# Optimization experiments

Hardware: AMD Instinct MI355X
Metric: run time of the kernel (lower is better)

Reference implementation:

```python
import jax, jax.numpy as jnp
import numpy as np

B, LQ, LK, D, H, DFF = 2, 2048, 2048, 512, 8, 2048


def _xavier(key, shape):
    fan_in, fan_out = shape[0], shape[1]
    lim = float(np.sqrt(6.0 / (fan_in + fan_out)))
    return jax.random.uniform(key, shape, jnp.float32, -lim, lim)


def setup_inputs() -> dict:
    key = jax.random.key(0)
    ks = jax.random.split(key, 8)
    return {
        "inputs": jax.random.normal(ks[0], (B, LQ, D), jnp.float32),
        "encoder_x": jax.random.normal(ks[1], (B, LK, D), jnp.float32),
        "Wq": _xavier(ks[2], (D, D)),
        "Wk": _xavier(ks[3], (D, D)),
        "Wv": _xavier(ks[4], (D, D)),
        "ln1_g": jnp.ones((D,), jnp.float32),
        "ln1_b": jnp.zeros((D,), jnp.float32),
        "W1": jax.random.normal(ks[5], (D, DFF), jnp.float32) * 0.02,
        "b1": jnp.zeros((DFF,), jnp.float32),
        "W2": jax.random.normal(ks[6], (DFF, D), jnp.float32) * 0.02,
        "b2": jnp.zeros((D,), jnp.float32),
        "ln2_g": jnp.ones((D,), jnp.float32),
        "ln2_b": jnp.zeros((D,), jnp.float32),
        "n_heads": H,
    }


def _layer_norm(x, g, b, eps=1e-5):
    mu = jnp.mean(x, axis=-1, keepdims=True)
    var = jnp.var(x, axis=-1, keepdims=True)
    return (x - mu) * jax.lax.rsqrt(var + eps) * g + b


def reference(inputs, encoder_x, Wq, Wk, Wv, ln1_g, ln1_b, W1, b1, W2, b2, ln2_g, ln2_b, n_heads):
    b, lq, d = inputs.shape
    lk = encoder_x.shape[1]
    hd = d // n_heads
    q = (inputs @ Wq).reshape(b, lq, n_heads, hd)
    k = (encoder_x @ Wk).reshape(b, lk, n_heads, hd)
    v = (encoder_x @ Wv).reshape(b, lk, n_heads, hd)
    # scores: [b, h, lq, lk]; scale by sqrt(head_dim) as in source
    scores = jnp.einsum("bqhd,bkhd->bhqk", q, k) / jnp.sqrt(jnp.asarray(hd, q.dtype))
    attn = jax.nn.softmax(scores, axis=-1)
    o = jnp.einsum("bhqk,bkhd->bqhd", attn, v).reshape(b, lq, d)
    out = _layer_norm(o + inputs, ln1_g, ln1_b)
    ff = jax.nn.relu(out @ W1 + b1) @ W2 + b2
    return _layer_norm(ff + out, ln2_g, ln2_b)
```

## Files before the change

kernel.cpp:

```cpp
#include <hip/hip_runtime.h>

typedef __bf16 bf16_t;
typedef __bf16 bf16x8 __attribute__((ext_vector_type(8)));
typedef __bf16 bf16x4 __attribute__((ext_vector_type(4)));
typedef float f32x4 __attribute__((ext_vector_type(4)));
typedef float f32x16 __attribute__((ext_vector_type(16)));
typedef unsigned int u32;
typedef unsigned int u32x2 __attribute__((ext_vector_type(2)));

#define GLB_AS(p) ((const __attribute__((address_space(1))) unsigned int*)(p))
#define LDS_AS(p) ((__attribute__((address_space(3))) unsigned int*)(p))

#define SPLIT_ROWS 32768
#define KLD 68
#define VLD 44

__global__ void prep_kernel(const float* __restrict__ inputs, bf16_t* __restrict__ Xb, float scaleQ,
                            const float* __restrict__ encx, bf16_t* __restrict__ Eb,
                            const float* __restrict__ Wq, const float* __restrict__ Wk,
                            const float* __restrict__ Wv, const float* __restrict__ W1,
                            const float* __restrict__ W2, bf16_t* __restrict__ Wqkvt,
                            bf16_t* __restrict__ W1t, bf16_t* __restrict__ W2t)
{
    __shared__ float tile[32][33];
    const int bid = blockIdx.x;
    const int tid = threadIdx.x;
    if (bid < 4096) {
        const float* in;
        bf16_t* out;
        float scale;
        int i;
        if (bid < 2048) { in = inputs; out = Xb; scale = scaleQ; i = (bid * 256 + tid) * 4; }
        else            { in = encx;   out = Eb; scale = 1.0f;   i = ((bid - 2048) * 256 + tid) * 4; }
        float4 v = *(const float4*)(in + i);
        bf16x4 o;
        o[0] = (bf16_t)(v.x * scale); o[1] = (bf16_t)(v.y * scale);
        o[2] = (bf16_t)(v.z * scale); o[3] = (bf16_t)(v.w * scale);
        *(bf16x4*)(out + i) = o;
        return;
    }
    const int j = bid - 4096;
    const float* in;
    bf16_t* out;
    int R, C, bx, by;
    if (j < 768) {
        int k = j >> 8, l = j & 255;
        in = (k == 0) ? Wq : (k == 1) ? Wk : Wv;
        out = Wqkvt + k * 512 * 512;
        R = 512; C = 512; bx = l & 15; by = l >> 4;
    } else if (j < 1792) {
        int l = j - 768;
        in = W1; out = W1t; R = 512; C = 2048; bx = l % 64; by = l / 64;
    } else {
        int l = j - 1792;
        in = W2; out = W2t; R = 2048; C = 512; bx = l % 16; by = l / 16;
    }
    const int r0 = by * 32, c0 = bx * 32;
#pragma unroll
    for (int t = 0; t < 4; t++) {
        int r = t * 8 + (tid >> 5), c = tid & 31;
        tile[r][c] = in[(size_t)(r0 + r) * C + c0 + c];
    }
    __syncthreads();
#pragma unroll
    for (int t = 0; t < 4; t++) {
        int c = t * 8 + (tid >> 5), r = tid & 31;
        out[(size_t)(c0 + c) * R + r0 + r] = (bf16_t)tile[r][c];
    }
}

template<int BM, int BN, bool SPLITA, bool VFUSE, bool BIAS, bool RELU, bool OUTBF16>
__global__ __launch_bounds__(256)
void gemm_kernel(const bf16_t* __restrict__ A0, const bf16_t* __restrict__ A1, int nsplit,
                 const bf16_t* __restrict__ Bt, const float* __restrict__ bias,
                 void* __restrict__ Cout, bf16_t* __restrict__ VtOut, int K, int ldC)
{
    constexpr int FR = BM / 32, FC = BN / 32;
    __shared__ __align__(16) bf16_t As[2][BM * 32];
    __shared__ __align__(16) bf16_t Bs[2][BN * 32];
    const int bm = blockIdx.x, bn = blockIdx.y;
    const bf16_t* A = (!SPLITA || bn < nsplit) ? A0 : A1;
    const int tid = threadIdx.x;
    const int lane = tid & 63;
    const int wid = tid >> 6;
    const int wr = wid >> 1, wc = wid & 1;

    f32x4 acc[FR][FC] = {};

    const int cb = wid * 2;
    const int lbB0 = (BN == 128 ? cb * 1024 : wid * 1024) + lane * 16;
    const int rowB0 = lbB0 >> 6, colB0 = (lbB0 & 63) >> 1;
    const int rowB1 = (lbB0 + 1024) >> 6, colB1 = ((lbB0 + 1024) & 63) >> 1;
    const int lbA0 = (BM == 128 ? cb * 1024 : wid * 1024) + lane * 16;
    const int rowA0 = lbA0 >> 6, colA0 = (lbA0 & 63) >> 1;
    const int rowA1 = (lbA0 + 1024) >> 6, colA1 = ((lbA0 + 1024) & 63) >> 1;

    const bf16_t* Abase = A + (size_t)(bm * BM) * K;
    const bf16_t* Bbase = Bt + (size_t)(bn * BN) * K;

    auto stage = [&](int k0, int b_) {
        if constexpr (BM == 128) {
            __builtin_amdgcn_global_load_lds(GLB_AS(Abase + (size_t)rowA0 * K + k0 + colA0), LDS_AS(&As[b_][cb * 512]), 16, 0, 0);
            __builtin_amdgcn_global_load_lds(GLB_AS(Abase + (size_t)rowA1 * K + k0 + colA1), LDS_AS(&As[b_][cb * 512 + 512]), 16, 0, 0);
        } else {
            __builtin_amdgcn_global_load_lds(GLB_AS(Abase + (size_t)rowA0 * K + k0 + colA0), LDS_AS(&As[b_][wid * 512]), 16, 0, 0);
        }
        if constexpr (BN == 128) {
            __builtin_amdgcn_global_load_lds(GLB_AS(Bbase + (size_t)rowB0 * K + k0 + colB0), LDS_AS(&Bs[b_][cb * 512]), 16, 0, 0);
            __builtin_amdgcn_global_load_lds(GLB_AS(Bbase + (size_t)rowB1 * K + k0 + colB1), LDS_AS(&Bs[b_][cb * 512 + 512]), 16, 0, 0);
        } else {
            __builtin_amdgcn_global_load_lds(GLB_AS(Bbase + (size_t)rowB0 * K + k0 + colB0), LDS_AS(&Bs[b_][wid * 512]), 16, 0, 0);
        }
    };

    stage(0, 0);
    __syncthreads();

    int cur = 0;
    for (int k0 = 0; k0 < K; k0 += 32) {
        if (k0 + 32 < K) stage(k0 + 32, cur ^ 1);

        bf16x8 af[FR], bfr[FC];
#pragma unroll
        for (int f = 0; f < FR; f++)
            af[f] = *(const bf16x8*)&As[cur][(wr * (BM / 2) + f * 16 + (lane & 15)) * 32 + (lane >> 4) * 8];
#pragma unroll
        for (int f = 0; f < FC; f++)
            bfr[f] = *(const bf16x8*)&Bs[cur][(wc * (BN / 2) + f * 16 + (lane & 15)) * 32 + (lane >> 4) * 8];
#pragma unroll
        for (int fr = 0; fr < FR; fr++)
#pragma unroll
            for (int fc = 0; fc < FC; fc++)
                acc[fr][fc] = __builtin_amdgcn_mfma_f32_16x16x32_bf16(af[fr], bfr[fc], acc[fr][fc], 0, 0, 0);

        __syncthreads();
        cur ^= 1;
    }

    const int rg = (lane >> 4) * 4, cl = lane & 15;
    if (VFUSE && bn >= 8) {
#pragma unroll
        for (int fc = 0; fc < FC; fc++) {
            const int colv = (bn - 8) * BN + wc * (BN / 2) + fc * 16 + cl;
            const int h = colv >> 6, d = colv & 63;
#pragma unroll
            for (int fr = 0; fr < FR; fr++) {
                const int rowg = bm * BM + wr * (BM / 2) + fr * 16 + rg;
                const int b = rowg >> 11, lk = rowg & 2047;
                bf16x4 o;
#pragma unroll
                for (int r = 0; r < 4; r++) o[r] = (bf16_t)acc[fr][fc][r];
                *(bf16x4*)(VtOut + ((size_t)(b * 8 + h) * 64 + d) * 2048 + lk) = o;
            }
        }
        return;
    }
#pragma unroll
    for (int fc = 0; fc < FC; fc++) {
        const int col = bn * BN + wc * (BN / 2) + fc * 16 + cl;
        float bv = 0.f;
        if (BIAS) bv = bias[col];
#pragma unroll
        for (int fr = 0; fr < FR; fr++) {
#pragma unroll
            for (int r = 0; r < 4; r++) {
                int rowg = bm * BM + wr * (BM / 2) + fr * 16 + rg + r;
                float v = acc[fr][fc][r] + bv;
                if (RELU) v = fmaxf(v, 0.f);
                if (OUTBF16) ((bf16_t*)Cout)[(size_t)rowg * ldC + col] = (bf16_t)v;
                else         ((float*)Cout)[(size_t)rowg * ldC + col] = v;
            }
        }
    }
}

union BU { bf16x8 v; u32 d[4]; };

static __device__ __forceinline__ u32 pkbf(float a, float b)
{
    union { bf16_t h[2]; u32 w; } u;
    u.h[0] = (bf16_t)a; u.h[1] = (bf16_t)b;
    return u.w;
}

static __device__ __forceinline__ void plswap(u32 a, u32 b, u32& x, u32& y)
{
#if __has_builtin(__builtin_amdgcn_permlane32_swap)
    u32x2 r = __builtin_amdgcn_permlane32_swap(a, b, false, false);
    x = r[0]; y = r[1];
#else
    const bool hi = (threadIdx.x & 32) != 0;
    u32 sb = __shfl_xor(b, 32), sa = __shfl_xor(a, 32);
    x = hi ? sb : a;
    y = hi ? b : sa;
#endif
}

__global__ __launch_bounds__(256)
void flash_kernel(const bf16_t* __restrict__ QK, const bf16_t* __restrict__ Vt,
                  bf16_t* __restrict__ Op01, bf16_t* __restrict__ Op23,
                  float2* __restrict__ ml)
{
    const int tid = threadIdx.x, lane = tid & 63, wid = tid >> 6;
    const int bh = blockIdx.y, b = bh >> 3, h = bh & 7;
    const int split = blockIdx.z;
    const int qbase = blockIdx.x * 128 + wid * 32;
    const int l31 = lane & 31, hi = lane >> 5;

    __shared__ __align__(16) bf16_t Kst[2][32 * KLD];
    __shared__ __align__(16) bf16_t Vst[2][64 * VLD];
    __shared__ __align__(16) bf16_t tlds[4][32 * 68];
    bf16_t* tw = &tlds[wid][0];

    const bf16_t* Qp = QK + (size_t)(b * 2048 + qbase + l31) * 1024 + h * 64 + hi * 8;
    const bf16_t* Kbase = QK + (size_t)(b * 2048) * 1024 + 512 + h * 64;
    const bf16_t* Vbase = Vt + (size_t)bh * 64 * 2048;

    const int kr = tid >> 3, kc = (tid & 7) * 8;
    const int vr = tid >> 2, vc = (tid & 3) * 8;

    bf16x8 qf[4];
#pragma unroll
    for (int t = 0; t < 4; t++)
        qf[t] = *(const bf16x8*)(Qp + t * 16);

    bf16x8 ones;
#pragma unroll
    for (int e = 0; e < 8; e++) ones[e] = (bf16_t)1.0f;

    f32x16 acc0 = {}, acc1 = {}, accS = {};
    float mrun = -1e30f;

    const int kv0 = split * 512;

    bf16x8 kreg = *(const bf16x8*)(Kbase + (size_t)(kv0 + kr) * 1024 + kc);
    bf16x8 vreg = *(const bf16x8*)(Vbase + (size_t)vr * 2048 + kv0 + vc);
    *(bf16x8*)&Kst[0][kr * KLD + kc] = kreg;
    *(bf16x8*)&Vst[0][vr * VLD + vc] = vreg;
    __syncthreads();

    int buf = 0;
#pragma unroll 2
    for (int kt = kv0; kt < kv0 + 512; kt += 32) {
        const bool nxt = (kt + 32 < kv0 + 512);
        if (nxt) {
            kreg = *(const bf16x8*)(Kbase + (size_t)(kt + 32 + kr) * 1024 + kc);
            vreg = *(const bf16x8*)(Vbase + (size_t)vr * 2048 + kt + 32 + vc);
        }

        bf16x8 kf[4];
#pragma unroll
        for (int t = 0; t < 4; t++)
            kf[t] = *(const bf16x8*)&Kst[buf][l31 * KLD + hi * 8 + t * 16];
        bf16x8 vf00 = *(const bf16x8*)&Vst[buf][l31 * VLD + hi * 8];
        bf16x8 vf01 = *(const bf16x8*)&Vst[buf][l31 * VLD + 16 + hi * 8];
        bf16x8 vf10 = *(const bf16x8*)&Vst[buf][(32 + l31) * VLD + hi * 8];
        bf16x8 vf11 = *(const bf16x8*)&Vst[buf][(32 + l31) * VLD + 16 + hi * 8];

        f32x16 p = {};
        __builtin_amdgcn_s_setprio(1);
        p = __builtin_amdgcn_mfma_f32_32x32x16_bf16(kf[0], qf[0], p, 0, 0, 0);
        p = __builtin_amdgcn_mfma_f32_32x32x16_bf16(kf[1], qf[1], p, 0, 0, 0);
        p = __builtin_amdgcn_mfma_f32_32x32x16_bf16(kf[2], qf[2], p, 0, 0, 0);
        p = __builtin_amdgcn_mfma_f32_32x32x16_bf16(kf[3], qf[3], p, 0, 0, 0);
        __builtin_amdgcn_s_setprio(0);

        float x0 = fmaxf(p[0], p[8]),  x1 = fmaxf(p[1], p[9]);
        float x2 = fmaxf(p[2], p[10]), x3 = fmaxf(p[3], p[11]);
        float x4 = fmaxf(p[4], p[12]), x5 = fmaxf(p[5], p[13]);
        float x6 = fmaxf(p[6], p[14]), x7 = fmaxf(p[7], p[15]);
        x0 = fmaxf(x0, x4); x1 = fmaxf(x1, x5); x2 = fmaxf(x2, x6); x3 = fmaxf(x3, x7);
        float cm = fmaxf(fmaxf(x0, x1), fmaxf(x2, x3));
        {
            u32 r0, r1;
            plswap(__float_as_uint(cm), __float_as_uint(cm), r0, r1);
            cm = fmaxf(__uint_as_float(r0), __uint_as_float(r1));
        }

        if (__any(cm > mrun + 12.0f)) {
            float mnew = fmaxf(mrun, cm);
            float fac = __builtin_amdgcn_exp2f(mrun - mnew);
#pragma unroll
            for (int i = 0; i < 16; i++) { acc0[i] *= fac; acc1[i] *= fac; accS[i] *= fac; }
            mrun = mnew;
        }

        float e[16];
#pragma unroll
        for (int i = 0; i < 16; i++) e[i] = __builtin_amdgcn_exp2f(p[i] - mrun);

        u32 pk0 = pkbf(e[0], e[1]),   pk1 = pkbf(e[2], e[3]);
        u32 pk2 = pkbf(e[4], e[5]),   pk3 = pkbf(e[6], e[7]);
        u32 pk4 = pkbf(e[8], e[9]),   pk5 = pkbf(e[10], e[11]);
        u32 pk6 = pkbf(e[12], e[13]), pk7 = pkbf(e[14], e[15]);
        BU b0, b1;
        plswap(pk0, pk2, b0.d[0], b0.d[2]);
        plswap(pk1, pk3, b0.d[1], b0.d[3]);
        plswap(pk4, pk6, b1.d[0], b1.d[2]);
        plswap(pk5, pk7, b1.d[1], b1.d[3]);

        __builtin_amdgcn_s_setprio(1);
        acc0 = __builtin_amdgcn_mfma_f32_32x32x16_bf16(vf00, b0.v, acc0, 0, 0, 0);
        acc0 = __builtin_amdgcn_mfma_f32_32x32x16_bf16(vf01, b1.v, acc0, 0, 0, 0);
        acc1 = __builtin_amdgcn_mfma_f32_32x32x16_bf16(vf10, b0.v, acc1, 0, 0, 0);
        acc1 = __builtin_amdgcn_mfma_f32_32x32x16_bf16(vf11, b1.v, acc1, 0, 0, 0);
        accS = __builtin_amdgcn_mfma_f32_32x32x16_bf16(ones, b0.v, accS, 0, 0, 0);
        accS = __builtin_amdgcn_mfma_f32_32x32x16_bf16(ones, b1.v, accS, 0, 0, 0);
        __builtin_amdgcn_s_setprio(0);

        if (nxt) {
            *(bf16x8*)&Kst[buf ^ 1][kr * KLD + kc] = kreg;
            *(bf16x8*)&Vst[buf ^ 1][vr * VLD + vc] = vreg;
        }
        __syncthreads();
        buf ^= 1;
    }

    const float lsum = accS[0];
    float inv = 1.f / lsum;
#pragma unroll
    for (int r = 0; r < 16; r++) {
        int drow = (r & 3) + 8 * (r >> 2) + 4 * hi;
        tw[l31 * 68 + drow]      = (bf16_t)(acc0[r] * inv);
        tw[l31 * 68 + 32 + drow] = (bf16_t)(acc1[r] * inv);
    }
    bf16_t* Op = (split < 2) ? Op01 + (size_t)split * SPLIT_ROWS * 64
                             : Op23 + (size_t)(split - 2) * SPLIT_ROWS * 64;
    const size_t rowbase = (size_t)bh * 2048 + qbase;
#pragma unroll
    for (int ps = 0; ps < 4; ps++) {
        int rr = (lane >> 3) + ps * 8;
        int cc = lane & 7;
        bf16x8 ov = *(const bf16x8*)&tw[rr * 68 + cc * 8];
        *(bf16x8*)(Op + (rowbase + rr) * 64 + cc * 8) = ov;
    }
    if (lane < 32)
        ml[(size_t)split * SPLIT_ROWS + rowbase + l31] = make_float2(mrun, lsum);
}

__global__ __launch_bounds__(128)
void combine_ln_kernel(const bf16_t* __restrict__ Op01, const bf16_t* __restrict__ Op23,
                       const float2* __restrict__ ml, const float* __restrict__ resid,
                       const float* __restrict__ g, const float* __restrict__ bta,
                       bf16_t* __restrict__ outb)
{
    const int row = blockIdx.x;
    const int tid = threadIdx.x;
    const int b = row >> 11, q = row & 2047;
    const int d = tid * 4, h = d >> 6, dd = d & 63;
    const size_t prow = ((size_t)(b * 8 + h)) * 2048 + q;

    float2 m0 = ml[prow];
    float2 m1 = ml[SPLIT_ROWS + prow];
    float2 m2 = ml[2 * SPLIT_ROWS + prow];
    float2 m3 = ml[3 * SPLIT_ROWS + prow];
    float M = fmaxf(fmaxf(m0.x, m1.x), fmaxf(m2.x, m3.x));
    float w0 = m0.y * __builtin_amdgcn_exp2f(m0.x - M);
    float w1 = m1.y * __builtin_amdgcn_exp2f(m1.x - M);
    float w2 = m2.y * __builtin_amdgcn_exp2f(m2.x - M);
    float w3 = m3.y * __builtin_amdgcn_exp2f(m3.x - M);
    float winv = 1.f / (w0 + w1 + w2 + w3);

    bf16x4 p0 = *(const bf16x4*)(Op01 + prow * 64 + dd);
    bf16x4 p1 = *(const bf16x4*)(Op01 + (SPLIT_ROWS + prow) * 64 + dd);
    bf16x4 p2 = *(const bf16x4*)(Op23 + prow * 64 + dd);
    bf16x4 p3 = *(const bf16x4*)(Op23 + (SPLIT_ROWS + prow) * 64 + dd);
    float4 rv = ((const float4*)resid)[row * 128 + tid];

    float x0 = (w0 * (float)p0[0] + w1 * (float)p1[0] + w2 * (float)p2[0] + w3 * (float)p3[0]) * winv + rv.x;
    float x1 = (w0 * (float)p0[1] + w1 * (float)p1[1] + w2 * (float)p2[1] + w3 * (float)p3[1]) * winv + rv.y;
    float x2 = (w0 * (float)p0[2] + w1 * (float)p1[2] + w2 * (float)p2[2] + w3 * (float)p3[2]) * winv + rv.z;
    float x3 = (w0 * (float)p0[3] + w1 * (float)p1[3] + w2 * (float)p2[3] + w3 * (float)p3[3]) * winv + rv.w;

    float s = x0 + x1 + x2 + x3;
    float sq = x0 * x0 + x1 * x1 + x2 * x2 + x3 * x3;
#pragma unroll
    for (int dl = 1; dl < 64; dl <<= 1) { s += __shfl_xor(s, dl); sq += __shfl_xor(sq, dl); }
    __shared__ float red[2][2];
    const int wid = tid >> 6;
    if ((tid & 63) == 0) { red[wid][0] = s; red[wid][1] = sq; }
    __syncthreads();
    s = red[0][0] + red[1][0];
    sq = red[0][1] + red[1][1];
    float mu = s * (1.f / 512.f);
    float var = sq * (1.f / 512.f) - mu * mu;
    float rstd = rsqrtf(var + 1e-5f);
    const float4 gv = ((const float4*)g)[tid];
    const float4 bv = ((const float4*)bta)[tid];
    bf16x4 o;
    o[0] = (bf16_t)((x0 - mu) * rstd * gv.x + bv.x);
    o[1] = (bf16_t)((x1 - mu) * rstd * gv.y + bv.y);
    o[2] = (bf16_t)((x2 - mu) * rstd * gv.z + bv.z);
    o[3] = (bf16_t)((x3 - mu) * rstd * gv.w + bv.w);
    *(bf16x4*)(outb + (size_t)row * 512 + tid * 4) = o;
}

template<bool RESBF>
__global__ __launch_bounds__(128)
void add_ln_kernel(const float* __restrict__ a, const void* __restrict__ res,
                   const float* __restrict__ g, const float* __restrict__ bta,
                   float* outf, bf16_t* outb)
{
    const int row = blockIdx.x, tid = threadIdx.x;
    const float4* a4 = (const float4*)(a + (size_t)row * 512);
    float4 av = a4[tid];
    float r0, r1, r2, r3;
    if (RESBF) {
        bf16x4 rv = ((const bf16x4*)res)[row * 128 + tid];
        r0 = (float)rv[0]; r1 = (float)rv[1]; r2 = (float)rv[2]; r3 = (float)rv[3];
    } else {
        float4 rv = ((const float4*)res)[row * 128 + tid];
        r0 = rv.x; r1 = rv.y; r2 = rv.z; r3 = rv.w;
    }
    float x0 = av.x + r0, x1 = av.y + r1, x2 = av.z + r2, x3 = av.w + r3;
    float s = x0 + x1 + x2 + x3;
    float sq = x0 * x0 + x1 * x1 + x2 * x2 + x3 * x3;
#pragma unroll
    for (int d = 1; d < 64; d <<= 1) { s += __shfl_xor(s, d); sq += __shfl_xor(sq, d); }
    __shared__ float red[2][2];
    const int wid = tid >> 6;
    if ((tid & 63) == 0) { red[wid][0] = s; red[wid][1] = sq; }
    __syncthreads();
    s = red[0][0] + red[1][0];
    sq = red[0][1] + red[1][1];
    float mu = s * (1.f / 512.f);
    float var = sq * (1.f / 512.f) - mu * mu;
    float rstd = rsqrtf(var + 1e-5f);
    const float4* g4 = (const float4*)g;
    const float4* b4 = (const float4*)bta;
    float4 gv = g4[tid], bv = b4[tid];
    float4 y;
    y.x = (x0 - mu) * rstd * gv.x + bv.x;
    y.y = (x1 - mu) * rstd * gv.y + bv.y;
    y.z = (x2 - mu) * rstd * gv.z + bv.z;
    y.w = (x3 - mu) * rstd * gv.w + bv.w;
    if (outf) ((float4*)(outf + (size_t)row * 512))[tid] = y;
    if (outb) {
        bf16x4 o;
        o[0] = (bf16_t)y.x; o[1] = (bf16_t)y.y; o[2] = (bf16_t)y.z; o[3] = (bf16_t)y.w;
        *(bf16x4*)(outb + (size_t)row * 512 + tid * 4) = o;
    }
}

extern "C" void kernel_launch(void* const* d_in, const int* in_sizes, int n_in,
                              void* d_out, int out_size, void* d_ws, size_t ws_size,
                              hipStream_t stream)
{
    const float* inputs = (const float*)d_in[0];
    const float* encx   = (const float*)d_in[1];
    const float* Wq     = (const float*)d_in[2];
    const float* Wk     = (const float*)d_in[3];
    const float* Wv     = (const float*)d_in[4];
    const float* ln1g   = (const float*)d_in[5];
    const float* ln1b   = (const float*)d_in[6];
    const float* W1     = (const float*)d_in[7];
    const float* b1     = (const float*)d_in[8];
    const float* W2     = (const float*)d_in[9];
    const float* b2     = (const float*)d_in[10];
    const float* ln2g   = (const float*)d_in[11];
    const float* ln2b   = (const float*)d_in[12];

    char* ws = (char*)d_ws;
    const size_t MB = 1u << 20;
    bf16_t* W1t   = (bf16_t*)(ws);
    bf16_t* W2t   = (bf16_t*)(ws + 2 * MB);
    bf16_t* Xb    = (bf16_t*)(ws + 4 * MB);
    bf16_t* Op01  = (bf16_t*)(ws + 4 * MB);
    bf16_t* Hb    = (bf16_t*)(ws + 4 * MB);
    bf16_t* Eb    = (bf16_t*)(ws + 8 * MB);
    bf16_t* QKb   = (bf16_t*)(ws + 12 * MB);
    bf16_t* Vtb   = (bf16_t*)(ws + 24 * MB);
    bf16_t* out1b = (bf16_t*)(ws + 24 * MB);
    bf16_t* Wqkvt = (bf16_t*)(ws + 28 * MB);
    float2* mlbuf = (float2*)(ws + 28 * MB);
    bf16_t* Op23  = (bf16_t*)d_out;
    float*  FF    = (float*)d_out;

    prep_kernel<<<6912, 256, 0, stream>>>(inputs, Xb, 0.125f * 1.44269504f, encx, Eb,
                                          Wq, Wk, Wv, W1, W2, Wqkvt, W1t, W2t);
    gemm_kernel<64, 128, true, true, false, false, true><<<dim3(64, 12), 256, 0, stream>>>(
        Xb, Eb, 4, Wqkvt, nullptr, QKb, Vtb, 512, 1024);
    flash_kernel<<<dim3(16, 16, 4), 256, 0, stream>>>(QKb, Vtb, Op01, Op23, mlbuf);
    combine_ln_kernel<<<4096, 128, 0, stream>>>(Op01, Op23, mlbuf, inputs, ln1g, ln1b, out1b);
    gemm_kernel<128, 128, false, false, true, true, true><<<dim3(32, 16), 256, 0, stream>>>(
        out1b, nullptr, 0, W1t, b1, Hb, nullptr, 512, 2048);
    gemm_kernel<64, 64, false, false, true, false, false><<<dim3(64, 8), 256, 0, stream>>>(
        Hb, nullptr, 0, W2t, b2, FF, nullptr, 2048, 512);
    add_ln_kernel<true><<<4096, 128, 0, stream>>>(FF, out1b, ln2g, ln2b, (float*)d_out, nullptr);
}
```

Before: 121.0 us.

## Swizzle flash block order, drop setprio, emit FFN output as bf16

The flash kernel now launches on a 1D grid and remaps block indices so that consecutive physical blocks are spread across logical (q-block, head, split) tiles, which is meant to improve XCD/L2 locality for shared K/V. The s_setprio hints around the MFMA groups are removed. The second FFN GEMM now writes bf16 into a workspace buffer instead of fp32 into the output, and the final add+layernorm reads bf16 for both operands. This halves that intermediate's memory traffic but adds rounding error before the last layernorm.

New measurement: 117.2 us. 3.2% less time.

```diff
diff --git a/kernel.cpp b/kernel.cpp
--- a/kernel.cpp
+++ b/kernel.cpp
@@ -202,9 +202,11 @@
                   float2* __restrict__ ml)
 {
     const int tid = threadIdx.x, lane = tid & 63, wid = tid >> 6;
-    const int bh = blockIdx.y, b = bh >> 3, h = bh & 7;
-    const int split = blockIdx.z;
-    const int qbase = blockIdx.x * 128 + wid * 32;
+    const int phys = blockIdx.x;
+    const int logical = (phys & 7) * 128 + (phys >> 3);
+    const int qb = logical & 15, bh = (logical >> 4) & 15, split = logical >> 8;
+    const int b = bh >> 3, h = bh & 7;
+    const int qbase = qb * 128 + wid * 32;
     const int l31 = lane & 31, hi = lane >> 5;
 
     __shared__ __align__(16) bf16_t Kst[2][32 * KLD];
@@ -258,12 +260,10 @@
         bf16x8 vf11 = *(const bf16x8*)&Vst[buf][(32 + l31) * VLD + 16 + hi * 8];
 
         f32x16 p = {};
-        __builtin_amdgcn_s_setprio(1);
         p = __builtin_amdgcn_mfma_f32_32x32x16_bf16(kf[0], qf[0], p, 0, 0, 0);
         p = __builtin_amdgcn_mfma_f32_32x32x16_bf16(kf[1], qf[1], p, 0, 0, 0);
         p = __builtin_amdgcn_mfma_f32_32x32x16_bf16(kf[2], qf[2], p, 0, 0, 0);
         p = __builtin_amdgcn_mfma_f32_32x32x16_bf16(kf[3], qf[3], p, 0, 0, 0);
-        __builtin_amdgcn_s_setprio(0);
 
         float x0 = fmaxf(p[0], p[8]),  x1 = fmaxf(p[1], p[9]);
         float x2 = fmaxf(p[2], p[10]), x3 = fmaxf(p[3], p[11]);
@@ -299,14 +299,12 @@
         plswap(pk4, pk6, b1.d[0], b1.d[2]);
         plswap(pk5, pk7, b1.d[1], b1.d[3]);
 
-        __builtin_amdgcn_s_setprio(1);
         acc0 = __builtin_amdgcn_mfma_f32_32x32x16_bf16(vf00, b0.v, acc0, 0, 0, 0);
         acc0 = __builtin_amdgcn_mfma_f32_32x32x16_bf16(vf01, b1.v, acc0, 0, 0, 0);
         acc1 = __builtin_amdgcn_mfma_f32_32x32x16_bf16(vf10, b0.v, acc1, 0, 0, 0);
         acc1 = __builtin_amdgcn_mfma_f32_32x32x16_bf16(vf11, b1.v, acc1, 0, 0, 0);
         accS = __builtin_amdgcn_mfma_f32_32x32x16_bf16(ones, b0.v, accS, 0, 0, 0);
         accS = __builtin_amdgcn_mfma_f32_32x32x16_bf16(ones, b1.v, accS, 0, 0, 0);
-        __builtin_amdgcn_s_setprio(0);
 
         if (nxt) {
             *(bf16x8*)&Kst[buf ^ 1][kr * KLD + kc] = kreg;
@@ -395,24 +393,18 @@
     *(bf16x4*)(outb + (size_t)row * 512 + tid * 4) = o;
 }
 
-template<bool RESBF>
 __global__ __launch_bounds__(128)
-void add_ln_kernel(const float* __restrict__ a, const void* __restrict__ res,
+void add_ln_kernel(const bf16_t* __restrict__ a, const bf16_t* __restrict__ res,
                    const float* __restrict__ g, const float* __restrict__ bta,
-                   float* outf, bf16_t* outb)
+                   float* __restrict__ outf)
 {
     const int row = blockIdx.x, tid = threadIdx.x;
-    const float4* a4 = (const float4*)(a + (size_t)row * 512);
-    float4 av = a4[tid];
-    float r0, r1, r2, r3;
-    if (RESBF) {
-        bf16x4 rv = ((const bf16x4*)res)[row * 128 + tid];
-        r0 = (float)rv[0]; r1 = (float)rv[1]; r2 = (float)rv[2]; r3 = (float)rv[3];
-    } else {
-        float4 rv = ((const float4*)res)[row * 128 + tid];
-        r0 = rv.x; r1 = rv.y; r2 = rv.z; r3 = rv.w;
-    }
-    float x0 = av.x + r0, x1 = av.y + r1, x2 = av.z + r2, x3 = av.w + r3;
+    bf16x4 av = ((const bf16x4*)a)[row * 128 + tid];
+    bf16x4 rv = ((const bf16x4*)res)[row * 128 + tid];
+    float x0 = (float)av[0] + (float)rv[0];
+    float x1 = (float)av[1] + (float)rv[1];
+    float x2 = (float)av[2] + (float)rv[2];
+    float x3 = (float)av[3] + (float)rv[3];
     float s = x0 + x1 + x2 + x3;
     float sq = x0 * x0 + x1 * x1 + x2 * x2 + x3 * x3;
 #pragma unroll
@@ -426,20 +418,14 @@
     float mu = s * (1.f / 512.f);
     float var = sq * (1.f / 512.f) - mu * mu;
     float rstd = rsqrtf(var + 1e-5f);
-    const float4* g4 = (const float4*)g;
-    const float4* b4 = (const float4*)bta;
-    float4 gv = g4[tid], bv = b4[tid];
+    const float4 gv = ((const float4*)g)[tid];
+    const float4 bv = ((const float4*)bta)[tid];
     float4 y;
     y.x = (x0 - mu) * rstd * gv.x + bv.x;
     y.y = (x1 - mu) * rstd * gv.y + bv.y;
     y.z = (x2 - mu) * rstd * gv.z + bv.z;
     y.w = (x3 - mu) * rstd * gv.w + bv.w;
-    if (outf) ((float4*)(outf + (size_t)row * 512))[tid] = y;
-    if (outb) {
-        bf16x4 o;
-        o[0] = (bf16_t)y.x; o[1] = (bf16_t)y.y; o[2] = (bf16_t)y.z; o[3] = (bf16_t)y.w;
-        *(bf16x4*)(outb + (size_t)row * 512 + tid * 4) = o;
-    }
+    ((float4*)(outf + (size_t)row * 512))[tid] = y;
 }
 
 extern "C" void kernel_launch(void* const* d_in, const int* in_sizes, int n_in,
@@ -469,22 +455,22 @@
     bf16_t* Hb    = (bf16_t*)(ws + 4 * MB);
     bf16_t* Eb    = (bf16_t*)(ws + 8 * MB);
     bf16_t* QKb   = (bf16_t*)(ws + 12 * MB);
+    bf16_t* FFb   = (bf16_t*)(ws + 20 * MB);
     bf16_t* Vtb   = (bf16_t*)(ws + 24 * MB);
     bf16_t* out1b = (bf16_t*)(ws + 24 * MB);
     bf16_t* Wqkvt = (bf16_t*)(ws + 28 * MB);
     float2* mlbuf = (float2*)(ws + 28 * MB);
     bf16_t* Op23  = (bf16_t*)d_out;
-    float*  FF    = (float*)d_out;
 
     prep_kernel<<<6912, 256, 0, stream>>>(inputs, Xb, 0.125f * 1.44269504f, encx, Eb,
                                           Wq, Wk, Wv, W1, W2, Wqkvt, W1t, W2t);
     gemm_kernel<64, 128, true, true, false, false, true><<<dim3(64, 12), 256, 0, stream>>>(
         Xb, Eb, 4, Wqkvt, nullptr, QKb, Vtb, 512, 1024);
-    flash_kernel<<<dim3(16, 16, 4), 256, 0, stream>>>(QKb, Vtb, Op01, Op23, mlbuf);
+    flash_kernel<<<1024, 256, 0, stream>>>(QKb, Vtb, Op01, Op23, mlbuf);
     combine_ln_kernel<<<4096, 128, 0, stream>>>(Op01, Op23, mlbuf, inputs, ln1g, ln1b, out1b);
     gemm_kernel<128, 128, false, false, true, true, true><<<dim3(32, 16), 256, 0, stream>>>(
         out1b, nullptr, 0, W1t, b1, Hb, nullptr, 512, 2048);
-    gemm_kernel<64, 64, false, false, true, false, false><<<dim3(64, 8), 256, 0, stream>>>(
-        Hb, nullptr, 0, W2t, b2, FF, nullptr, 2048, 512);
-    add_ln_kernel<true><<<4096, 128, 0, stream>>>(FF, out1b, ln2g, ln2b, (float*)d_out, nullptr);
-}
+    gemm_kernel<64, 64, false, false, true, false, true><<<dim3(64, 8), 256, 0, stream>>>(
+        Hb, nullptr, 0, W2t, b2, FFb, nullptr, 2048, 512);
+    add_ln_kernel<<<4096, 128, 0, stream>>>(FFb, out1b, ln2g, ln2b, (float*)d_out);
+}
```
